# Kernel tuning notes

Measured on AMD Instinct MI355X. Metric: run time of the kernel, lower is better.

The kernel has to match this reference:

```python
import jax, jax.numpy as jnp
import numpy as np

N_NODES = 20000
N_EDGES = 640000
D = 64        # node / edge feature dim
H = 128       # MLP hidden dim


def setup_inputs() -> dict:
    key = jax.random.key(0)
    ks = jax.random.split(key, 12)
    inp = {
        "x": jax.random.normal(ks[0], (N_NODES, D), dtype=jnp.float32),
        "edge_index": jax.random.randint(ks[1], (2, N_EDGES), 0, N_NODES, dtype=jnp.int64),
        "edge_attr": jax.random.normal(ks[2], (N_EDGES, D), dtype=jnp.float32),
        "f": jax.random.normal(ks[3], (N_NODES, D), dtype=jnp.float32),
        # edge MLP: concat(x_src, x_dest, edge_attr) = 3D -> H -> D
        "We1": jax.random.normal(ks[4], (3 * D, H), dtype=jnp.float32) / np.sqrt(3 * D),
        "be1": jnp.zeros((H,), dtype=jnp.float32),
        "We2": jax.random.normal(ks[5], (H, D), dtype=jnp.float32) / np.sqrt(H),
        "be2": jnp.zeros((D,), dtype=jnp.float32),
        # node MLP: concat(x, agg, f) = 3D -> H -> D
        "Wn1": jax.random.normal(ks[6], (3 * D, H), dtype=jnp.float32) / np.sqrt(3 * D),
        "bn1": jnp.zeros((H,), dtype=jnp.float32),
        "Wn2": jax.random.normal(ks[7], (H, D), dtype=jnp.float32) / np.sqrt(H),
        "bn2": jnp.zeros((D,), dtype=jnp.float32),
    }
    return inp


def reference(x, edge_index, edge_attr, f, We1, be1, We2, be2, Wn1, bn1, Wn2, bn2):
    src, dest = edge_index[0], edge_index[1]
    # edge model: MLP over gathered src/dest node features + edge attrs
    e_in = jnp.concatenate([x[src], x[dest], edge_attr], axis=-1)      # [E, 3D]
    e_h = jax.nn.relu(e_in @ We1 + be1)                                 # [E, H]
    edge_out = e_h @ We2 + be2                                          # [E, D]
    # node model: scatter-add edge messages to dest, then MLP
    agg = jax.ops.segment_sum(edge_out, dest, num_segments=N_NODES)    # [N, D]
    n_in = jnp.concatenate([x, agg, f], axis=-1)                        # [N, 3D]
    n_h = jax.nn.relu(n_in @ Wn1 + bn1)                                 # [N, H]
    x_out = n_h @ Wn2 + bn2                                             # [N, D]
    return (x_out, edge_out)
```

## Files before the change

kernel.cpp:

```cpp
#include <hip/hip_runtime.h>

#define NE 640000
#define NN 20000
#define SEI 200
#define SEH 136

typedef __attribute__((ext_vector_type(8))) short s16x8;
typedef __attribute__((ext_vector_type(4))) short s16x4;
typedef __attribute__((ext_vector_type(4))) float f32x4;

__device__ __forceinline__ short f2bf(float f) {
  unsigned int u = __float_as_uint(f);
  u += 0x7fffu + ((u >> 16) & 1u);
  return (short)(u >> 16);
}

__device__ __forceinline__ s16x8 cvt8(f32x4 a, f32x4 b) {
  s16x8 o;
  o[0]=f2bf(a[0]); o[1]=f2bf(a[1]); o[2]=f2bf(a[2]); o[3]=f2bf(a[3]);
  o[4]=f2bf(b[0]); o[5]=f2bf(b[1]); o[6]=f2bf(b[2]); o[7]=f2bf(b[3]);
  return o;
}

__device__ __forceinline__ void load_wfrags(const float* W1, const float* W2,
                                            const float* b1, const float* b2,
                                            int wv, int r, int g,
                                            s16x8 w1f[2][6], s16x8 w2f[4],
                                            f32x4 b1r[2], f32x4* b2r) {
  #pragma unroll
  for (int nn = 0; nn < 2; ++nn) {
    const int h = (wv*2+nn)*16 + r;
    #pragma unroll
    for (int kk = 0; kk < 6; ++kk) {
      s16x8 wf;
      #pragma unroll
      for (int i = 0; i < 8; ++i)
        wf[i] = f2bf(W1[(size_t)(kk*32 + g*8 + i)*128 + h]);
      w1f[nn][kk] = wf;
    }
    b1r[nn] = *(const f32x4*)(b1 + (wv*2+nn)*16 + g*4);
  }
  const int h2 = wv*16 + r;
  #pragma unroll
  for (int kk = 0; kk < 4; ++kk) {
    s16x8 wf;
    #pragma unroll
    for (int i = 0; i < 8; ++i)
      wf[i] = f2bf(W2[(size_t)(kk*32 + g*8 + i)*64 + h2]);
    w2f[kk] = wf;
  }
  *b2r = *(const f32x4*)(b2 + wv*16 + g*4);
}


__global__ void count_kernel(const int* __restrict__ eidx, int* __restrict__ cursor) {
  for (int e = blockIdx.x * blockDim.x + threadIdx.x; e < NE;
       e += gridDim.x * blockDim.x)
    atomicAdd(&cursor[eidx[NE + e]], 1);
}

__global__ __launch_bounds__(1024)
void scan_kernel(int* __restrict__ cursor, int* __restrict__ offs) {
  __shared__ int part[1024];
  const int t = threadIdx.x;
  const int CH = 20;
  const int lo = t * CH, hi = min(lo + CH, NN);
  int s = 0;
  for (int i = lo; i < hi; ++i) s += cursor[i];
  part[t] = s;
  __syncthreads();
  for (int d = 1; d < 1024; d <<= 1) {
    int u = (t >= d) ? part[t - d] : 0;
    __syncthreads();
    part[t] += u;
    __syncthreads();
  }
  int run = part[t] - s;
  for (int i = lo; i < hi; ++i) {
    int c = cursor[i];
    offs[i] = run;
    cursor[i] = run;
    run += c;
  }
  if (t == 1023) offs[NN] = NE;
}

__global__ void scatter_kernel(const int* __restrict__ eidx,
                               int* __restrict__ cursor, int* __restrict__ elist) {
  for (int e = blockIdx.x * blockDim.x + threadIdx.x; e < NE;
       e += gridDim.x * blockDim.x) {
    int pos = atomicAdd(&cursor[eidx[NE + e]], 1);
    elist[pos] = e;
  }
}

#define LOAD_ROWS(sv, dv, ee) do {                                        \
    const f32x4* ps_ = (const f32x4*)(x  + (size_t)(sv)*64 + p*16);       \
    const f32x4* pd_ = (const f32x4*)(x  + (size_t)(dv)*64 + p*16);       \
    const f32x4* pe_ = (const f32x4*)(ea + (size_t)(ee)*64 + p*16);       \
    L[0]=ps_[0]; L[1]=ps_[1]; L[2]=ps_[2];  L[3]=ps_[3];                  \
    L[4]=pd_[0]; L[5]=pd_[1]; L[6]=pd_[2];  L[7]=pd_[3];                  \
    L[8]=pe_[0]; L[9]=pe_[1]; L[10]=pe_[2]; L[11]=pe_[3];                 \
  } while (0)

#define WRITE_EIN(buf) do {                                               \
    short* stg_ = (buf) + el*SEI + p*16;                                  \
    ((s16x8*)stg_)[0]       = cvt8(L[0], L[1]);                           \
    ((s16x8*)stg_)[1]       = cvt8(L[2], L[3]);                           \
    ((s16x8*)(stg_+64))[0]  = cvt8(L[4], L[5]);                           \
    ((s16x8*)(stg_+64))[1]  = cvt8(L[6], L[7]);                           \
    ((s16x8*)(stg_+128))[0] = cvt8(L[8], L[9]);                           \
    ((s16x8*)(stg_+128))[1] = cvt8(L[10], L[11]);                         \
  } while (0)

__global__ __launch_bounds__(256, 2)
void edge_kernel(const float* __restrict__ x, const int* __restrict__ eidx,
                 const float* __restrict__ ea,
                 const float* __restrict__ We1, const float* __restrict__ be1,
                 const float* __restrict__ We2, const float* __restrict__ be2,
                 float* __restrict__ edge_out)
{
  __shared__ __align__(16) short sEin[2][64 * SEI];
  __shared__ __align__(16) short sEh[64 * SEH];

  const int t = threadIdx.x;
  const int wv = t >> 6, lane = t & 63;
  const int r = lane & 15, g = lane >> 4;

  s16x8 w1f[2][6], w2f[4];
  f32x4 b1r[2], b2r;
  load_wfrags(We1, We2, be1, be2, wv, r, g, w1f, w2f, b1r, &b2r);

  const int el = t >> 2, p = t & 3;
  const int nT = NE / 64;
  const int S = (int)gridDim.x;
  const f32x4 zero = {0.f, 0.f, 0.f, 0.f};

  f32x4 L[12];
  int sN = 0, dN = 0;
  int tile = blockIdx.x;

  if (tile < nT) {
    int e = (tile << 6) + el;
    int sv = eidx[e], dv = eidx[NE + e];
    LOAD_ROWS(sv, dv, e);
    WRITE_EIN(sEin[0]);
    const int t1 = tile + S;
    if (t1 < nT) {
      e = (t1 << 6) + el;
      sv = eidx[e]; dv = eidx[NE + e];
      LOAD_ROWS(sv, dv, e);
    }
    const int t2 = tile + 2 * S;
    if (t2 < nT) { e = (t2 << 6) + el; sN = eidx[e]; dN = eidx[NE + e]; }
  }
  __syncthreads();

  int cur = 0;
  while (tile < nT) {
    const int tW = tile + S, tI = tile + 2 * S, tX = tile + 3 * S;
    if (tW < nT) WRITE_EIN(sEin[cur ^ 1]);
    if (tI < nT) { const int e = (tI << 6) + el; LOAD_ROWS(sN, dN, e); }
    if (tX < nT) { const int e = (tX << 6) + el; sN = eidx[e]; dN = eidx[NE + e]; }

    const short* Ecur = sEin[cur];
    f32x4 acc1[2][4];
    #pragma unroll
    for (int nn = 0; nn < 2; ++nn)
      #pragma unroll
      for (int j = 0; j < 4; ++j) acc1[nn][j] = zero;
    #pragma unroll
    for (int kk = 0; kk < 6; ++kk) {
      #pragma unroll
      for (int j = 0; j < 4; ++j) {
        s16x8 ef = *(const s16x8*)&Ecur[(j*16 + r)*SEI + kk*32 + g*8];
        acc1[0][j] = __builtin_amdgcn_mfma_f32_16x16x32_bf16(w1f[0][kk], ef, acc1[0][j], 0, 0, 0);
        acc1[1][j] = __builtin_amdgcn_mfma_f32_16x16x32_bf16(w1f[1][kk], ef, acc1[1][j], 0, 0, 0);
      }
    }
    #pragma unroll
    for (int nn = 0; nn < 2; ++nn)
      #pragma unroll
      for (int j = 0; j < 4; ++j) {
        s16x4 pk;
        #pragma unroll
        for (int q = 0; q < 4; ++q) {
          float v = acc1[nn][j][q] + b1r[nn][q];
          pk[q] = f2bf(v > 0.f ? v : 0.f);
        }
        *(s16x4*)&sEh[(j*16 + r)*SEH + (wv*2+nn)*16 + g*4] = pk;
      }
    __syncthreads();

    const int ebase = tile << 6;
    #pragma unroll
    for (int j = 0; j < 4; ++j) {
      f32x4 a2 = zero;
      #pragma unroll
      for (int kk = 0; kk < 4; ++kk) {
        s16x8 hf = *(const s16x8*)&sEh[(j*16 + r)*SEH + kk*32 + g*8];
        a2 = __builtin_amdgcn_mfma_f32_16x16x32_bf16(w2f[kk], hf, a2, 0, 0, 0);
      }
      f32x4 v = a2 + b2r;
      *(f32x4*)&edge_out[(size_t)(ebase + j*16 + r)*64 + wv*16 + g*4] = v;
    }
    __syncthreads();
    cur ^= 1;
    tile += S;
  }
}

__global__ __launch_bounds__(256)
void agg_kernel(const float* __restrict__ eo, const int* __restrict__ offs,
                const int* __restrict__ elist, float* __restrict__ agg) {
  const int w = threadIdx.x >> 6;
  const int lane = threadIdx.x & 63;
  for (int i = blockIdx.x * 4 + w; i < NN; i += (int)gridDim.x * 4) {
    int j = offs[i];
    const int end = offs[i + 1];
    float acc0 = 0.f, acc1 = 0.f;
    for (; j + 8 <= end; j += 8) {
      int e0 = elist[j],   e1 = elist[j+1], e2 = elist[j+2], e3 = elist[j+3];
      int e4 = elist[j+4], e5 = elist[j+5], e6 = elist[j+6], e7 = elist[j+7];
      float v0 = eo[(size_t)e0*64 + lane];
      float v1 = eo[(size_t)e1*64 + lane];
      float v2 = eo[(size_t)e2*64 + lane];
      float v3 = eo[(size_t)e3*64 + lane];
      float v4 = eo[(size_t)e4*64 + lane];
      float v5 = eo[(size_t)e5*64 + lane];
      float v6 = eo[(size_t)e6*64 + lane];
      float v7 = eo[(size_t)e7*64 + lane];
      acc0 += (v0 + v1) + (v2 + v3);
      acc1 += (v4 + v5) + (v6 + v7);
    }
    for (; j < end; ++j) acc0 += eo[(size_t)elist[j]*64 + lane];
    agg[(size_t)i*64 + lane] = acc0 + acc1;
  }
}

__global__ __launch_bounds__(256, 2)
void node_kernel(const float* __restrict__ x, const float* agg,
                 const float* __restrict__ f,
                 const float* __restrict__ Wn1, const float* __restrict__ bn1,
                 const float* __restrict__ Wn2, const float* __restrict__ bn2,
                 float* x_out)
{
  __shared__ __align__(16) short sEin1[64 * SEI];
  __shared__ __align__(16) short sEh[64 * SEH];

  const int t = threadIdx.x;
  const int wv = t >> 6, lane = t & 63;
  const int r = lane & 15, g = lane >> 4;

  s16x8 w1f[2][6], w2f[4];
  f32x4 b1r[2], b2r;
  load_wfrags(Wn1, Wn2, bn1, bn2, wv, r, g, w1f, w2f, b1r, &b2r);

  const int el = t >> 2, p = t & 3;
  const f32x4 zero = {0.f, 0.f, 0.f, 0.f};
  const int base = blockIdx.x << 6;
  const int i = base + el;

  f32x4 L[12];
  if (i < NN) {
    const f32x4* ps_ = (const f32x4*)(x   + (size_t)i*64 + p*16);
    const f32x4* pa_ = (const f32x4*)(agg + (size_t)i*64 + p*16);
    const f32x4* pf_ = (const f32x4*)(f   + (size_t)i*64 + p*16);
    L[0]=ps_[0]; L[1]=ps_[1]; L[2]=ps_[2];  L[3]=ps_[3];
    L[4]=pa_[0]; L[5]=pa_[1]; L[6]=pa_[2];  L[7]=pa_[3];
    L[8]=pf_[0]; L[9]=pf_[1]; L[10]=pf_[2]; L[11]=pf_[3];
  } else {
    #pragma unroll
    for (int q = 0; q < 12; ++q) L[q] = zero;
  }
  {
    short* stg_ = sEin1 + el*SEI + p*16;
    ((s16x8*)stg_)[0]       = cvt8(L[0], L[1]);
    ((s16x8*)stg_)[1]       = cvt8(L[2], L[3]);
    ((s16x8*)(stg_+64))[0]  = cvt8(L[4], L[5]);
    ((s16x8*)(stg_+64))[1]  = cvt8(L[6], L[7]);
    ((s16x8*)(stg_+128))[0] = cvt8(L[8], L[9]);
    ((s16x8*)(stg_+128))[1] = cvt8(L[10], L[11]);
  }
  __syncthreads();

  f32x4 acc1[2][4];
  #pragma unroll
  for (int nn = 0; nn < 2; ++nn)
    #pragma unroll
    for (int j = 0; j < 4; ++j) acc1[nn][j] = zero;
  #pragma unroll
  for (int kk = 0; kk < 6; ++kk) {
    #pragma unroll
    for (int j = 0; j < 4; ++j) {
      s16x8 ef = *(const s16x8*)&sEin1[(j*16 + r)*SEI + kk*32 + g*8];
      acc1[0][j] = __builtin_amdgcn_mfma_f32_16x16x32_bf16(w1f[0][kk], ef, acc1[0][j], 0, 0, 0);
      acc1[1][j] = __builtin_amdgcn_mfma_f32_16x16x32_bf16(w1f[1][kk], ef, acc1[1][j], 0, 0, 0);
    }
  }
  #pragma unroll
  for (int nn = 0; nn < 2; ++nn)
    #pragma unroll
    for (int j = 0; j < 4; ++j) {
      s16x4 pk;
      #pragma unroll
      for (int q = 0; q < 4; ++q) {
        float v = acc1[nn][j][q] + b1r[nn][q];
        pk[q] = f2bf(v > 0.f ? v : 0.f);
      }
      *(s16x4*)&sEh[(j*16 + r)*SEH + (wv*2+nn)*16 + g*4] = pk;
    }
  __syncthreads();

  #pragma unroll
  for (int j = 0; j < 4; ++j) {
    f32x4 a2 = zero;
    #pragma unroll
    for (int kk = 0; kk < 4; ++kk) {
      s16x8 hf = *(const s16x8*)&sEh[(j*16 + r)*SEH + kk*32 + g*8];
      a2 = __builtin_amdgcn_mfma_f32_16x16x32_bf16(w2f[kk], hf, a2, 0, 0, 0);
    }
    const int row = base + j*16 + r;
    if (row < NN) {
      f32x4 v = a2 + b2r;
      *(f32x4*)&x_out[(size_t)row*64 + wv*16 + g*4] = v;
    }
  }
}

extern "C" void kernel_launch(void* const* d_in, const int* in_sizes, int n_in,
                              void* d_out, int out_size, void* d_ws, size_t ws_size,
                              hipStream_t stream) {
  const float* x   = (const float*)d_in[0];
  const int*   ei  = (const int*)d_in[1];
  const float* ea  = (const float*)d_in[2];
  const float* f   = (const float*)d_in[3];
  const float* We1 = (const float*)d_in[4];
  const float* be1 = (const float*)d_in[5];
  const float* We2 = (const float*)d_in[6];
  const float* be2 = (const float*)d_in[7];
  const float* Wn1 = (const float*)d_in[8];
  const float* bn1 = (const float*)d_in[9];
  const float* Wn2 = (const float*)d_in[10];
  const float* bn2 = (const float*)d_in[11];

  float* x_out    = (float*)d_out;
  float* edge_out = x_out + (size_t)NN * 64;

  int* cursor = (int*)d_ws;
  int* offs   = cursor + NN;
  int* elist  = offs + NN + 8;

  hipMemsetAsync(cursor, 0, NN * sizeof(int), stream);
  count_kernel<<<1024, 256, 0, stream>>>(ei, cursor);
  scan_kernel<<<1, 1024, 0, stream>>>(cursor, offs);
  scatter_kernel<<<1024, 256, 0, stream>>>(ei, cursor, elist);
  edge_kernel<<<512, 256, 0, stream>>>(x, ei, ea, We1, be1, We2, be2, edge_out);
  agg_kernel<<<1024, 256, 0, stream>>>(edge_out, offs, elist, x_out);
  node_kernel<<<313, 256, 0, stream>>>(x, x_out, f, Wn1, bn1, Wn2, bn2, x_out);
}
```

Measured before the change: 262.6 us.

## Stage weights through LDS, single-buffer edge input, and vectorize aggregation

Weights are loaded from global memory in coalesced float4 reads, converted to bf16 and staged in LDS before being gathered into MFMA fragments, where previously each lane did strided scalar global loads. The edge kernel drops its double-buffered input tile for a single buffer written after the first GEMM, which cuts LDS use enough to allow three blocks per CU and a 768-block grid. The aggregation kernel now has each wave handle four edges at a time with float4 lanes and reduces across lane groups with shuffles, and its grid doubles. Single buffering shortens the window in which the next tile's loads overlap compute, and the higher occupancy target may force register spills.

```diff
diff --git a/kernel.cpp b/kernel.cpp
--- a/kernel.cpp
+++ b/kernel.cpp
@@ -8,6 +8,8 @@
 typedef __attribute__((ext_vector_type(8))) short s16x8;
 typedef __attribute__((ext_vector_type(4))) short s16x4;
 typedef __attribute__((ext_vector_type(4))) float f32x4;
+
+typedef const __attribute__((ext_vector_type(4))) float cf32x4;
 
 __device__ __forceinline__ short f2bf(float f) {
   unsigned int u = __float_as_uint(f);
@@ -22,11 +24,20 @@
   return o;
 }
 
-__device__ __forceinline__ void load_wfrags(const float* W1, const float* W2,
-                                            const float* b1, const float* b2,
-                                            int wv, int r, int g,
-                                            s16x8 w1f[2][6], s16x8 w2f[4],
-                                            f32x4 b1r[2], f32x4* b2r) {
+__device__ __forceinline__ void load_wfrags_lds(const float* W1, const float* W2,
+                                                const float* b1, const float* b2,
+                                                short* smem, int t,
+                                                int wv, int r, int g,
+                                                s16x8 w1f[2][6], s16x8 w2f[4],
+                                                f32x4 b1r[2], f32x4* b2r) {
+  #pragma unroll
+  for (int i = 0; i < 24; ++i) {
+    int idx4 = t + i * 256;
+    f32x4 v = ((cf32x4*)W1)[idx4];
+    s16x4 pk; pk[0]=f2bf(v[0]); pk[1]=f2bf(v[1]); pk[2]=f2bf(v[2]); pk[3]=f2bf(v[3]);
+    *(s16x4*)&smem[idx4 * 4] = pk;
+  }
+  __syncthreads();
   #pragma unroll
   for (int nn = 0; nn < 2; ++nn) {
     const int h = (wv*2+nn)*16 + r;
@@ -34,22 +45,32 @@
     for (int kk = 0; kk < 6; ++kk) {
       s16x8 wf;
       #pragma unroll
-      for (int i = 0; i < 8; ++i)
-        wf[i] = f2bf(W1[(size_t)(kk*32 + g*8 + i)*128 + h]);
+      for (int i = 0; i < 8; ++i) wf[i] = smem[(kk*32 + g*8 + i)*128 + h];
       w1f[nn][kk] = wf;
     }
-    b1r[nn] = *(const f32x4*)(b1 + (wv*2+nn)*16 + g*4);
-  }
-  const int h2 = wv*16 + r;
-  #pragma unroll
-  for (int kk = 0; kk < 4; ++kk) {
-    s16x8 wf;
-    #pragma unroll
-    for (int i = 0; i < 8; ++i)
-      wf[i] = f2bf(W2[(size_t)(kk*32 + g*8 + i)*64 + h2]);
-    w2f[kk] = wf;
-  }
-  *b2r = *(const f32x4*)(b2 + wv*16 + g*4);
+    b1r[nn] = *(cf32x4*)(b1 + (wv*2+nn)*16 + g*4);
+  }
+  __syncthreads();
+  #pragma unroll
+  for (int i = 0; i < 8; ++i) {
+    int idx4 = t + i * 256;
+    f32x4 v = ((cf32x4*)W2)[idx4];
+    s16x4 pk; pk[0]=f2bf(v[0]); pk[1]=f2bf(v[1]); pk[2]=f2bf(v[2]); pk[3]=f2bf(v[3]);
+    *(s16x4*)&smem[idx4 * 4] = pk;
+  }
+  __syncthreads();
+  {
+    const int h2 = wv*16 + r;
+    #pragma unroll
+    for (int kk = 0; kk < 4; ++kk) {
+      s16x8 wf;
+      #pragma unroll
+      for (int i = 0; i < 8; ++i) wf[i] = smem[(kk*32 + g*8 + i)*64 + h2];
+      w2f[kk] = wf;
+    }
+    *b2r = *(cf32x4*)(b2 + wv*16 + g*4);
+  }
+  __syncthreads();
 }
 
 
@@ -95,9 +116,9 @@
 }
 
 #define LOAD_ROWS(sv, dv, ee) do {                                        \
-    const f32x4* ps_ = (const f32x4*)(x  + (size_t)(sv)*64 + p*16);       \
-    const f32x4* pd_ = (const f32x4*)(x  + (size_t)(dv)*64 + p*16);       \
-    const f32x4* pe_ = (const f32x4*)(ea + (size_t)(ee)*64 + p*16);       \
+    cf32x4* ps_ = (cf32x4*)(x  + (size_t)(sv)*64 + p*16);                 \
+    cf32x4* pd_ = (cf32x4*)(x  + (size_t)(dv)*64 + p*16);                 \
+    cf32x4* pe_ = (cf32x4*)(ea + (size_t)(ee)*64 + p*16);                 \
     L[0]=ps_[0]; L[1]=ps_[1]; L[2]=ps_[2];  L[3]=ps_[3];                  \
     L[4]=pd_[0]; L[5]=pd_[1]; L[6]=pd_[2];  L[7]=pd_[3];                  \
     L[8]=pe_[0]; L[9]=pe_[1]; L[10]=pe_[2]; L[11]=pe_[3];                 \
@@ -113,15 +134,16 @@
     ((s16x8*)(stg_+128))[1] = cvt8(L[10], L[11]);                         \
   } while (0)
 
-__global__ __launch_bounds__(256, 2)
+__global__ __launch_bounds__(256, 3)
 void edge_kernel(const float* __restrict__ x, const int* __restrict__ eidx,
                  const float* __restrict__ ea,
                  const float* __restrict__ We1, const float* __restrict__ be1,
                  const float* __restrict__ We2, const float* __restrict__ be2,
                  float* __restrict__ edge_out)
 {
-  __shared__ __align__(16) short sEin[2][64 * SEI];
-  __shared__ __align__(16) short sEh[64 * SEH];
+  __shared__ __align__(16) short smem[24576];
+  short* sEin = smem;
+  short* sEh  = smem + 12800;
 
   const int t = threadIdx.x;
   const int wv = t >> 6, lane = t & 63;
@@ -129,7 +151,7 @@
 
   s16x8 w1f[2][6], w2f[4];
   f32x4 b1r[2], b2r;
-  load_wfrags(We1, We2, be1, be2, wv, r, g, w1f, w2f, b1r, &b2r);
+  load_wfrags_lds(We1, We2, be1, be2, smem, t, wv, r, g, w1f, w2f, b1r, &b2r);
 
   const int el = t >> 2, p = t & 3;
   const int nT = NE / 64;
@@ -144,7 +166,7 @@
     int e = (tile << 6) + el;
     int sv = eidx[e], dv = eidx[NE + e];
     LOAD_ROWS(sv, dv, e);
-    WRITE_EIN(sEin[0]);
+    WRITE_EIN(sEin);
     const int t1 = tile + S;
     if (t1 < nT) {
       e = (t1 << 6) + el;
@@ -156,14 +178,7 @@
   }
   __syncthreads();
 
-  int cur = 0;
   while (tile < nT) {
-    const int tW = tile + S, tI = tile + 2 * S, tX = tile + 3 * S;
-    if (tW < nT) WRITE_EIN(sEin[cur ^ 1]);
-    if (tI < nT) { const int e = (tI << 6) + el; LOAD_ROWS(sN, dN, e); }
-    if (tX < nT) { const int e = (tX << 6) + el; sN = eidx[e]; dN = eidx[NE + e]; }
-
-    const short* Ecur = sEin[cur];
     f32x4 acc1[2][4];
     #pragma unroll
     for (int nn = 0; nn < 2; ++nn)
@@ -173,7 +188,7 @@
     for (int kk = 0; kk < 6; ++kk) {
       #pragma unroll
       for (int j = 0; j < 4; ++j) {
-        s16x8 ef = *(const s16x8*)&Ecur[(j*16 + r)*SEI + kk*32 + g*8];
+        s16x8 ef = *(const s16x8*)&sEin[(j*16 + r)*SEI + kk*32 + g*8];
         acc1[0][j] = __builtin_amdgcn_mfma_f32_16x16x32_bf16(w1f[0][kk], ef, acc1[0][j], 0, 0, 0);
         acc1[1][j] = __builtin_amdgcn_mfma_f32_16x16x32_bf16(w1f[1][kk], ef, acc1[1][j], 0, 0, 0);
       }
@@ -192,6 +207,11 @@
       }
     __syncthreads();
 
+    const int tW = tile + S, tI = tile + 2 * S, tX = tile + 3 * S;
+    if (tW < nT) WRITE_EIN(sEin);
+    if (tI < nT) { const int e = (tI << 6) + el; LOAD_ROWS(sN, dN, e); }
+    if (tX < nT) { const int e = (tX << 6) + el; sN = eidx[e]; dN = eidx[NE + e]; }
+
     const int ebase = tile << 6;
     #pragma unroll
     for (int j = 0; j < 4; ++j) {
@@ -205,7 +225,6 @@
       *(f32x4*)&edge_out[(size_t)(ebase + j*16 + r)*64 + wv*16 + g*4] = v;
     }
     __syncthreads();
-    cur ^= 1;
     tile += S;
   }
 }
@@ -215,38 +234,41 @@
                 const int* __restrict__ elist, float* __restrict__ agg) {
   const int w = threadIdx.x >> 6;
   const int lane = threadIdx.x & 63;
+  const int cg = lane & 15, rg = lane >> 4;
   for (int i = blockIdx.x * 4 + w; i < NN; i += (int)gridDim.x * 4) {
-    int j = offs[i];
     const int end = offs[i + 1];
-    float acc0 = 0.f, acc1 = 0.f;
-    for (; j + 8 <= end; j += 8) {
-      int e0 = elist[j],   e1 = elist[j+1], e2 = elist[j+2], e3 = elist[j+3];
-      int e4 = elist[j+4], e5 = elist[j+5], e6 = elist[j+6], e7 = elist[j+7];
-      float v0 = eo[(size_t)e0*64 + lane];
-      float v1 = eo[(size_t)e1*64 + lane];
-      float v2 = eo[(size_t)e2*64 + lane];
-      float v3 = eo[(size_t)e3*64 + lane];
-      float v4 = eo[(size_t)e4*64 + lane];
-      float v5 = eo[(size_t)e5*64 + lane];
-      float v6 = eo[(size_t)e6*64 + lane];
-      float v7 = eo[(size_t)e7*64 + lane];
-      acc0 += (v0 + v1) + (v2 + v3);
-      acc1 += (v4 + v5) + (v6 + v7);
-    }
-    for (; j < end; ++j) acc0 += eo[(size_t)elist[j]*64 + lane];
-    agg[(size_t)i*64 + lane] = acc0 + acc1;
-  }
-}
-
-__global__ __launch_bounds__(256, 2)
+    f32x4 a0 = {0.f,0.f,0.f,0.f}, a1 = {0.f,0.f,0.f,0.f};
+    int j = offs[i] + rg;
+    for (; j + 4 < end; j += 8) {
+      const int e0 = elist[j];
+      const int e1 = elist[j + 4];
+      a0 += *(cf32x4*)&eo[(size_t)e0*64 + cg*4];
+      a1 += *(cf32x4*)&eo[(size_t)e1*64 + cg*4];
+    }
+    if (j < end) {
+      const int e = elist[j];
+      a0 += *(cf32x4*)&eo[(size_t)e*64 + cg*4];
+    }
+    f32x4 a = a0 + a1;
+    #pragma unroll
+    for (int q = 0; q < 4; ++q) {
+      a[q] += __shfl_xor(a[q], 16);
+      a[q] += __shfl_xor(a[q], 32);
+    }
+    if (rg == 0) *(f32x4*)&agg[(size_t)i*64 + cg*4] = a;
+  }
+}
+
+__global__ __launch_bounds__(256, 3)
 void node_kernel(const float* __restrict__ x, const float* agg,
                  const float* __restrict__ f,
                  const float* __restrict__ Wn1, const float* __restrict__ bn1,
                  const float* __restrict__ Wn2, const float* __restrict__ bn2,
                  float* x_out)
 {
-  __shared__ __align__(16) short sEin1[64 * SEI];
-  __shared__ __align__(16) short sEh[64 * SEH];
+  __shared__ __align__(16) short smem[24576];
+  short* sEin = smem;
+  short* sEh  = smem + 12800;
 
   const int t = threadIdx.x;
   const int wv = t >> 6, lane = t & 63;
@@ -254,7 +276,7 @@
 
   s16x8 w1f[2][6], w2f[4];
   f32x4 b1r[2], b2r;
-  load_wfrags(Wn1, Wn2, bn1, bn2, wv, r, g, w1f, w2f, b1r, &b2r);
+  load_wfrags_lds(Wn1, Wn2, bn1, bn2, smem, t, wv, r, g, w1f, w2f, b1r, &b2r);
 
   const int el = t >> 2, p = t & 3;
   const f32x4 zero = {0.f, 0.f, 0.f, 0.f};
@@ -263,9 +285,9 @@
 
   f32x4 L[12];
   if (i < NN) {
-    const f32x4* ps_ = (const f32x4*)(x   + (size_t)i*64 + p*16);
-    const f32x4* pa_ = (const f32x4*)(agg + (size_t)i*64 + p*16);
-    const f32x4* pf_ = (const f32x4*)(f   + (size_t)i*64 + p*16);
+    cf32x4* ps_ = (cf32x4*)(x   + (size_t)i*64 + p*16);
+    cf32x4* pa_ = (cf32x4*)(agg + (size_t)i*64 + p*16);
+    cf32x4* pf_ = (cf32x4*)(f   + (size_t)i*64 + p*16);
     L[0]=ps_[0]; L[1]=ps_[1]; L[2]=ps_[2];  L[3]=ps_[3];
     L[4]=pa_[0]; L[5]=pa_[1]; L[6]=pa_[2];  L[7]=pa_[3];
     L[8]=pf_[0]; L[9]=pf_[1]; L[10]=pf_[2]; L[11]=pf_[3];
@@ -274,7 +296,7 @@
     for (int q = 0; q < 12; ++q) L[q] = zero;
   }
   {
-    short* stg_ = sEin1 + el*SEI + p*16;
+    short* stg_ = sEin + el*SEI + p*16;
     ((s16x8*)stg_)[0]       = cvt8(L[0], L[1]);
     ((s16x8*)stg_)[1]       = cvt8(L[2], L[3]);
     ((s16x8*)(stg_+64))[0]  = cvt8(L[4], L[5]);
@@ -293,7 +315,7 @@
   for (int kk = 0; kk < 6; ++kk) {
     #pragma unroll
     for (int j = 0; j < 4; ++j) {
-      s16x8 ef = *(const s16x8*)&sEin1[(j*16 + r)*SEI + kk*32 + g*8];
+      s16x8 ef = *(const s16x8*)&sEin[(j*16 + r)*SEI + kk*32 + g*8];
       acc1[0][j] = __builtin_amdgcn_mfma_f32_16x16x32_bf16(w1f[0][kk], ef, acc1[0][j], 0, 0, 0);
       acc1[1][j] = __builtin_amdgcn_mfma_f32_16x16x32_bf16(w1f[1][kk], ef, acc1[1][j], 0, 0, 0);
     }
@@ -355,7 +377,7 @@
   count_kernel<<<1024, 256, 0, stream>>>(ei, cursor);
   scan_kernel<<<1, 1024, 0, stream>>>(cursor, offs);
   scatter_kernel<<<1024, 256, 0, stream>>>(ei, cursor, elist);
-  edge_kernel<<<512, 256, 0, stream>>>(x, ei, ea, We1, be1, We2, be2, edge_out);
-  agg_kernel<<<1024, 256, 0, stream>>>(edge_out, offs, elist, x_out);
+  edge_kernel<<<768, 256, 0, stream>>>(x, ei, ea, We1, be1, We2, be2, edge_out);
+  agg_kernel<<<2048, 256, 0, stream>>>(edge_out, offs, elist, x_out);
   node_kernel<<<313, 256, 0, stream>>>(x, x_out, f, Wn1, bn1, Wn2, bn2, x_out);
 }
```

New measurement: 343.5 us. 1.31x slower.
